# Kernel optimization log

Hardware: AMD Instinct MI355X
Metric: run time of the kernel (lower is better)

Reference implementation:

```python
import jax, jax.numpy as jnp
import numpy as np

N, E = 50000, 600000
D_IN, HID, CLS = 128, 128, 64
TEM = (0.9, 0.8)  # tem[0], tem[1] from init


def setup_inputs() -> dict:
    key = jax.random.key(0)
    ks = jax.random.split(key, 20)
    def lin(k, fan_in, shape):
        return (jax.random.normal(k, shape, jnp.float32) / np.float32(np.sqrt(fan_in)))
    return {
        "features": jax.random.normal(ks[0], (N, D_IN), jnp.float32),
        "src1": jax.random.randint(ks[1], (E,), 0, N, jnp.int32),
        "dst1": jax.random.randint(ks[2], (E,), 0, N, jnp.int32),
        "src2": jax.random.randint(ks[3], (E,), 0, N, jnp.int32),
        "dst2": jax.random.randint(ks[4], (E,), 0, N, jnp.int32),
        "W1": lin(ks[5], D_IN, (D_IN, HID)),
        "b1": jnp.zeros((HID,), jnp.float32),
        "W2": lin(ks[6], HID, (HID, CLS)),
        "b2": jnp.zeros((CLS,), jnp.float32),
        "Wg11": lin(ks[7], 2 * HID, (2 * HID, 1)),
        "bg11": jnp.zeros((1,), jnp.float32),
        "Wg12": lin(ks[8], 2 * HID, (2 * HID, 1)),
        "bg12": jnp.zeros((1,), jnp.float32),
        "Wg21": lin(ks[9], 2 * CLS, (2 * CLS, 1)),
        "bg21": jnp.zeros((1,), jnp.float32),
        "Wg22": lin(ks[10], 2 * CLS, (2 * CLS, 1)),
        "bg22": jnp.zeros((1,), jnp.float32),
    }


def _gin(x, src, dst, W, b):
    # DGL GINConv, aggregator='sum', eps=0: apply_func(x + sum_{u->v} x_u)
    agg = jax.ops.segment_sum(x[src], dst, num_segments=N)  # [N, d]
    return (x + agg) @ W + b


def _gate_scale(a, c, Wg, bg):
    # ga = softmax(Linear(cat[a,c]), dim=1): [N,1] -> all ones (size-1 axis)
    # torch.diag of [N,1] matrix -> its single diagonal element [0,0]
    g = jnp.concatenate([a, c], axis=1) @ Wg + bg  # [N, 1]
    g = jax.nn.softmax(g, axis=1)
    return g[0, 0]  # scalar (dropout is identity in eval mode)


def reference(features, src1, dst1, src2, dst2, W1, b1, W2, b2,
              Wg11, bg11, Wg12, bg12, Wg21, bg21, Wg22, bg22):
    # layer 1 on both graphs (no ELU in the two-graph branch, per source)
    x11 = _gin(features, src1, dst1, W1, b1)
    x12 = _gin(features, src2, dst2, W1, b1)
    x12 = TEM[1] * _gate_scale(x11, x12, Wg11, bg11) * x12
    x11 = TEM[0] * _gate_scale(x12, x11, Wg12, bg12) * x11
    x1 = x11 + x12
    # layer 2 on both graphs
    x21 = _gin(x1, src1, dst1, W2, b2)
    x22 = _gin(x1, src2, dst2, W2, b2)
    x22 = TEM[1] * _gate_scale(x21, x22, Wg21, bg21) * x22
    x21 = TEM[0] * _gate_scale(x22, x21, Wg22, bg22) * x21
    return x21 + x22
```

## Files before the change

kernel.cpp:

```cpp
#include <hip/hip_runtime.h>

#define N_NODES 50000
#define N_EDGES 600000
#define D 128
#define NCLS 64

#define BIN_SHIFT 9
#define BIN_ROWS 512
#define NBINS 196
#define BIN_CAP 8192
#define CHUNK 4096
#define EPT (CHUNK / 256)
#define NCHUNKS 293
#define W12_BLOCKS 17

__device__ inline unsigned short f2bf(float f) {
  unsigned int u = __float_as_uint(f);
  unsigned int r = (u + 0x7FFF + ((u >> 16) & 1)) >> 16;
  return (unsigned short)r;
}
__device__ inline float bf2f(unsigned short b) {
  return __uint_as_float(((unsigned int)b) << 16);
}


__global__ __launch_bounds__(256) void scatter_w12(const int* __restrict__ src1,
                                                   const int* __restrict__ dst1,
                                                   const int* __restrict__ src2,
                                                   const int* __restrict__ dst2,
                                                   int* __restrict__ bincnt,
                                                   int2* __restrict__ binbuf,
                                                   const float* __restrict__ W1,
                                                   const float* __restrict__ W2,
                                                   const float* __restrict__ b1,
                                                   float* __restrict__ W12,
                                                   float* __restrict__ cvec) {
  __shared__ int bcnt[NBINS];
  __shared__ int boff[NBINS];
  __shared__ int gbase[NBINS];
  __shared__ int stmp[256];
  __shared__ int2 stage[CHUNK];

  if (blockIdx.x >= NCHUNKS) {
    int gid = (blockIdx.x - NCHUNKS) * 256 + threadIdx.x;
    for (int t = gid; t < D * NCLS + NCLS; t += W12_BLOCKS * 256) {
      if (t < D * NCLS) {
        int i = t >> 6, j = t & 63;
        float s = 0.f;
        for (int k = 0; k < D; ++k) s += W1[i * D + k] * W2[k * NCLS + j];
        W12[t] = s;
      } else {
        int j = t - D * NCLS;
        float s = 0.f;
        for (int k = 0; k < D; ++k) s += b1[k] * W2[k * NCLS + j];
        cvec[j] = s;
      }
    }
    return;
  }

  int base = blockIdx.x * CHUNK;
  int nloc = min(CHUNK, 2 * N_EDGES - base);

  for (int t = threadIdx.x; t < NBINS; t += 256) bcnt[t] = 0;
  __syncthreads();

  int rows[EPT], srcs[EPT], bins[EPT];
#pragma unroll
  for (int k = 0; k < EPT; ++k) {
    int t = threadIdx.x + k * 256;
    rows[k] = -1;
    if (t < nloc) {
      int i = base + t;
      int row, sv;
      if (i < N_EDGES) { row = dst1[i]; sv = src1[i]; }
      else { int e = i - N_EDGES; row = N_NODES + dst2[e]; sv = src2[e]; }
      rows[k] = row; srcs[k] = sv;
      bins[k] = row >> BIN_SHIFT;
      atomicAdd(&bcnt[bins[k]], 1);
    }
  }
  __syncthreads();
  {
    int tid = threadIdx.x;
    int v = (tid < NBINS) ? bcnt[tid] : 0;
    stmp[tid] = v;
    __syncthreads();
    int x = v;
    for (int o = 1; o < 256; o <<= 1) {
      int y = (tid >= o) ? stmp[tid - o] : 0;
      __syncthreads();
      x += y;
      stmp[tid] = x;
      __syncthreads();
    }
    if (tid < NBINS) boff[tid] = x - v;
  }
  __syncthreads();
  for (int t = threadIdx.x; t < NBINS; t += 256) {
    gbase[t] = bcnt[t];
    bcnt[t] = boff[t];
  }
  __syncthreads();
#pragma unroll
  for (int k = 0; k < EPT; ++k) {
    if (rows[k] >= 0) {
      int p = atomicAdd(&bcnt[bins[k]], 1);
      stage[p] = make_int2(rows[k], srcs[k]);
    }
  }
  __syncthreads();
  for (int t = threadIdx.x; t < NBINS; t += 256) {
    int c = gbase[t];
    if (c > 0) gbase[t] = atomicAdd(&bincnt[t], c);
  }
  __syncthreads();
  for (int j = threadIdx.x; j < nloc; j += 256) {
    int2 e = stage[j];
    int b = e.x >> BIN_SHIFT;
    int gp = gbase[b] + (j - boff[b]);
    if (gp < BIN_CAP) binbuf[(size_t)b * BIN_CAP + gp] = e;
  }
}


__global__ __launch_bounds__(512) void build_gemm(const int* __restrict__ bincnt,
                                                  const int2* __restrict__ binbuf,
                                                  int* __restrict__ off, int* __restrict__ adj,
                                                  const float* __restrict__ A,
                                                  const float* __restrict__ W,
                                                  unsigned short* __restrict__ C) {
  __shared__ int sh[BIN_ROWS];
  __shared__ int lp[BIN_ROWS];
  __shared__ int stmp[256];
  __shared__ float As[16][65];
  __shared__ float Ws[16][64];

  int tid = threadIdx.x;

  if (blockIdx.x < NBINS) {
    int b = blockIdx.x;
    if (tid < 256) stmp[tid] = (tid < NBINS) ? bincnt[tid] : 0;
    __syncthreads();
    int x = (tid < 256) ? stmp[tid] : 0;
    for (int o = 1; o < 256; o <<= 1) {
      int y = (tid < 256 && tid >= o) ? stmp[tid - o] : 0;
      __syncthreads();
      x += y;
      if (tid < 256) stmp[tid] = x;
      __syncthreads();
    }
    int base = (b == 0) ? 0 : stmp[b - 1];
    if (b == 0 && tid == 0) off[2 * N_NODES] = stmp[NBINS - 1];
    int n = min(bincnt[b], BIN_CAP);

    sh[tid] = 0;
    __syncthreads();
    for (int t = tid; t < n; t += 512) {
      int row = binbuf[(size_t)b * BIN_CAP + t].x;
      atomicAdd(&sh[row & (BIN_ROWS - 1)], 1);
    }
    __syncthreads();
    int v = sh[tid];
    int xx = v;
    for (int o = 1; o < BIN_ROWS; o <<= 1) {
      int y = (tid >= o) ? sh[tid - o] : 0;
      __syncthreads();
      xx += y;
      sh[tid] = xx;
      __syncthreads();
    }
    lp[tid] = xx - v;
    int row = (b << BIN_SHIFT) + tid;
    if (row < 2 * N_NODES) off[row] = base + lp[tid];
    __syncthreads();
    sh[tid] = lp[tid];
    __syncthreads();
    for (int t = tid; t < n; t += 512) {
      int2 e = binbuf[(size_t)b * BIN_CAP + t];
      int p = atomicAdd(&sh[e.x & (BIN_ROWS - 1)], 1);
      adj[base + p] = e.y;
    }
    return;
  }

  constexpr int BM = 64, BK = 16, BN = 64;
  constexpr int TCOL = BN / 16;
  const int tx = tid & 15;
  const int ty = (tid >> 4) & 15;
  const int row0 = (blockIdx.x - NBINS) * BM;
  float acc[4][TCOL];
#pragma unroll
  for (int r = 0; r < 4; ++r)
#pragma unroll
    for (int c = 0; c < TCOL; ++c) acc[r][c] = 0.f;

  for (int k0 = 0; k0 < D; k0 += BK) {
    if (tid < 256) {
      int r = tid >> 2;
      int kq = (tid & 3) << 2;
      int gr = row0 + r;
      float4 v = make_float4(0.f, 0.f, 0.f, 0.f);
      if (gr < N_NODES) v = *(const float4*)(A + (size_t)gr * D + k0 + kq);
      As[kq + 0][r] = v.x;
      As[kq + 1][r] = v.y;
      As[kq + 2][r] = v.z;
      As[kq + 3][r] = v.w;
    }
    if (tid < 256) {
      int k = tid >> 4;
      int c4 = (tid & 15) << 2;
      *(float4*)(&Ws[k][c4]) = *(const float4*)(W + (size_t)(k0 + k) * BN + c4);
    }
    __syncthreads();
    if (tid < 256) {
#pragma unroll
      for (int k = 0; k < BK; ++k) {
        float a[4];
#pragma unroll
        for (int r = 0; r < 4; ++r) a[r] = As[k][ty * 4 + r];
        float w[TCOL];
#pragma unroll
        for (int c = 0; c < TCOL; ++c) w[c] = Ws[k][tx * TCOL + c];
#pragma unroll
        for (int r = 0; r < 4; ++r)
#pragma unroll
          for (int c = 0; c < TCOL; ++c) acc[r][c] += a[r] * w[c];
      }
    }
    __syncthreads();
  }
  if (tid < 256) {
#pragma unroll
    for (int r = 0; r < 4; ++r) {
      int gr = row0 + ty * 4 + r;
      if (gr < N_NODES) {
        ushort4 pk;
        pk.x = f2bf(acc[r][0]);
        pk.y = f2bf(acc[r][1]);
        pk.z = f2bf(acc[r][2]);
        pk.w = f2bf(acc[r][3]);
        *(ushort4*)(C + (size_t)gr * BN + tx * TCOL) = pk;
      }
    }
  }
}


template <int FIN, int OUT_BF16>
__global__ __launch_bounds__(256) void agg64_kernel(const unsigned short* __restrict__ X,
                                                    const int* __restrict__ off,
                                                    const int* __restrict__ adj,
                                                    const float* __restrict__ cvec,
                                                    const float* __restrict__ b2,
                                                    void* __restrict__ Yv) {
  int wid = (blockIdx.x * blockDim.x + threadIdx.x) >> 6;
  if (wid >= N_NODES) return;
  int lane = threadIdx.x & 63;

  float self = bf2f(X[(size_t)wid * 64 + lane]);

  int s1 = off[wid], e1 = off[wid + 1];
  int s2 = off[N_NODES + wid], e2 = off[N_NODES + wid + 1];

  float acc[2];
#pragma unroll
  for (int g = 0; g < 2; ++g) {
    int s = g ? s2 : s1, e = g ? e2 : e1;
    float a0 = 0.f, a1 = 0.f, a2 = 0.f, a3 = 0.f;
    for (int base = s; base < e; base += 64) {
      int m = e - base;
      if (m > 64) m = 64;
      int idx = (lane < m) ? adj[base + lane] : 0;
      int i = 0;
      for (; i + 4 <= m; i += 4) {
        int n0 = __shfl(idx, i + 0);
        int n1 = __shfl(idx, i + 1);
        int n2 = __shfl(idx, i + 2);
        int n3 = __shfl(idx, i + 3);
        float f0 = bf2f(X[(size_t)n0 * 64 + lane]);
        float f1 = bf2f(X[(size_t)n1 * 64 + lane]);
        float f2 = bf2f(X[(size_t)n2 * 64 + lane]);
        float f3 = bf2f(X[(size_t)n3 * 64 + lane]);
        a0 += f0; a1 += f1; a2 += f2; a3 += f3;
      }
      for (; i < m; ++i) {
        int n0 = __shfl(idx, i);
        a0 += bf2f(X[(size_t)n0 * 64 + lane]);
      }
    }
    acc[g] = (a0 + a1) + (a2 + a3);
  }
  float y = 1.7f * self + 0.9f * acc[0] + 0.8f * acc[1];
  if (FIN) {
    float sv = 1.7f * (1.7f + 0.9f * (float)(e1 - s1) + 0.8f * (float)(e2 - s2));
    y += sv * cvec[lane] + 1.7f * b2[lane];
  }
  if (OUT_BF16) {
    ((unsigned short*)Yv)[(size_t)wid * 64 + lane] = f2bf(y);
  } else {
    ((float*)Yv)[(size_t)wid * 64 + lane] = y;
  }
}


extern "C" void kernel_launch(void* const* d_in, const int* in_sizes, int n_in,
                              void* d_out, int out_size, void* d_ws, size_t ws_size,
                              hipStream_t stream) {
  const float* F  = (const float*)d_in[0];
  const int* src1 = (const int*)d_in[1];
  const int* dst1 = (const int*)d_in[2];
  const int* src2 = (const int*)d_in[3];
  const int* dst2 = (const int*)d_in[4];
  const float* W1 = (const float*)d_in[5];
  const float* b1 = (const float*)d_in[6];
  const float* W2 = (const float*)d_in[7];
  const float* b2 = (const float*)d_in[8];
  float* out = (float*)d_out;

  char* ws = (char*)d_ws;
  auto aln = [](size_t x) { return (x + 255) & ~(size_t)255; };
  size_t o = 0;
  int* bincnt  = (int*)(ws + o); o = aln(o + (size_t)NBINS * 4);
  int* off     = (int*)(ws + o); o = aln(o + ((size_t)2 * N_NODES + 1) * 4);
  int2* binbuf = (int2*)(ws + o); o = aln(o + (size_t)NBINS * BIN_CAP * 8);
  int* adj     = (int*)(ws + o); o = aln(o + (size_t)2 * N_EDGES * 4);
  float* W12   = (float*)(ws + o); o = aln(o + (size_t)D * NCLS * 4);
  float* cvec  = (float*)(ws + o); o = aln(o + NCLS * 4);
  unsigned short* H = (unsigned short*)(ws + o); o = aln(o + (size_t)N_NODES * NCLS * 2);
  unsigned short* T = (unsigned short*)(ws + o); o = aln(o + (size_t)N_NODES * NCLS * 2);
  (void)ws_size;

  hipMemsetAsync(bincnt, 0, (size_t)NBINS * 4, stream);
  scatter_w12<<<NCHUNKS + W12_BLOCKS, 256, 0, stream>>>(src1, dst1, src2, dst2,
                                                        bincnt, binbuf, W1, W2, b1, W12, cvec);
  build_gemm<<<NBINS + (N_NODES + 63) / 64, 512, 0, stream>>>(bincnt, binbuf, off, adj,
                                                              F, W12, H);
  agg64_kernel<0, 1><<<N_NODES / 4, 256, 0, stream>>>(H, off, adj, cvec, b2, T);
  agg64_kernel<1, 0><<<N_NODES / 4, 256, 0, stream>>>(T, off, adj, cvec, b2, out);
}
```

Baseline: 211.2 us.

## Interleave graph CSR rows per node and merge aggregation loops

```diff
diff --git a/kernel.cpp b/kernel.cpp
--- a/kernel.cpp
+++ b/kernel.cpp
@@ -73,8 +73,8 @@
     if (t < nloc) {
       int i = base + t;
       int row, sv;
-      if (i < N_EDGES) { row = dst1[i]; sv = src1[i]; }
-      else { int e = i - N_EDGES; row = N_NODES + dst2[e]; sv = src2[e]; }
+      if (i < N_EDGES) { row = dst1[i] * 2; sv = src1[i]; }
+      else { int e = i - N_EDGES; row = dst2[e] * 2 + 1; sv = src2[e]; }
       rows[k] = row; srcs[k] = sv;
       bins[k] = row >> BIN_SHIFT;
       atomicAdd(&bcnt[bins[k]], 1);
@@ -260,40 +260,51 @@
 
   float self = bf2f(X[(size_t)wid * 64 + lane]);
 
-  int s1 = off[wid], e1 = off[wid + 1];
-  int s2 = off[N_NODES + wid], e2 = off[N_NODES + wid + 1];
-
-  float acc[2];
-#pragma unroll
-  for (int g = 0; g < 2; ++g) {
-    int s = g ? s2 : s1, e = g ? e2 : e1;
-    float a0 = 0.f, a1 = 0.f, a2 = 0.f, a3 = 0.f;
-    for (int base = s; base < e; base += 64) {
-      int m = e - base;
-      if (m > 64) m = 64;
-      int idx = (lane < m) ? adj[base + lane] : 0;
-      int i = 0;
-      for (; i + 4 <= m; i += 4) {
-        int n0 = __shfl(idx, i + 0);
-        int n1 = __shfl(idx, i + 1);
-        int n2 = __shfl(idx, i + 2);
-        int n3 = __shfl(idx, i + 3);
-        float f0 = bf2f(X[(size_t)n0 * 64 + lane]);
-        float f1 = bf2f(X[(size_t)n1 * 64 + lane]);
-        float f2 = bf2f(X[(size_t)n2 * 64 + lane]);
-        float f3 = bf2f(X[(size_t)n3 * 64 + lane]);
-        a0 += f0; a1 += f1; a2 += f2; a3 += f3;
-      }
-      for (; i < m; ++i) {
-        int n0 = __shfl(idx, i);
-        a0 += bf2f(X[(size_t)n0 * 64 + lane]);
-      }
-    }
-    acc[g] = (a0 + a1) + (a2 + a3);
-  }
-  float y = 1.7f * self + 0.9f * acc[0] + 0.8f * acc[1];
+  int s = off[2 * wid], mid = off[2 * wid + 1], e = off[2 * wid + 2];
+
+  float a0 = 0.f, a1 = 0.f, a2 = 0.f, a3 = 0.f;
+  float a4 = 0.f, a5 = 0.f, a6 = 0.f, a7 = 0.f;
+  for (int base = s; base < e; base += 64) {
+    int m = e - base;
+    if (m > 64) m = 64;
+    int idx = (lane < m) ? adj[base + lane] : 0;
+    int i = 0;
+    for (; i + 8 <= m; i += 8) {
+      int n0 = __shfl(idx, i + 0);
+      int n1 = __shfl(idx, i + 1);
+      int n2 = __shfl(idx, i + 2);
+      int n3 = __shfl(idx, i + 3);
+      int n4 = __shfl(idx, i + 4);
+      int n5 = __shfl(idx, i + 5);
+      int n6 = __shfl(idx, i + 6);
+      int n7 = __shfl(idx, i + 7);
+      float w0 = (base + i + 0 < mid) ? 0.9f : 0.8f;
+      float w1 = (base + i + 1 < mid) ? 0.9f : 0.8f;
+      float w2 = (base + i + 2 < mid) ? 0.9f : 0.8f;
+      float w3 = (base + i + 3 < mid) ? 0.9f : 0.8f;
+      float w4 = (base + i + 4 < mid) ? 0.9f : 0.8f;
+      float w5 = (base + i + 5 < mid) ? 0.9f : 0.8f;
+      float w6 = (base + i + 6 < mid) ? 0.9f : 0.8f;
+      float w7 = (base + i + 7 < mid) ? 0.9f : 0.8f;
+      a0 += w0 * bf2f(X[(size_t)n0 * 64 + lane]);
+      a1 += w1 * bf2f(X[(size_t)n1 * 64 + lane]);
+      a2 += w2 * bf2f(X[(size_t)n2 * 64 + lane]);
+      a3 += w3 * bf2f(X[(size_t)n3 * 64 + lane]);
+      a4 += w4 * bf2f(X[(size_t)n4 * 64 + lane]);
+      a5 += w5 * bf2f(X[(size_t)n5 * 64 + lane]);
+      a6 += w6 * bf2f(X[(size_t)n6 * 64 + lane]);
+      a7 += w7 * bf2f(X[(size_t)n7 * 64 + lane]);
+    }
+    for (; i < m; ++i) {
+      int n0 = __shfl(idx, i);
+      float w = (base + i < mid) ? 0.9f : 0.8f;
+      a0 += w * bf2f(X[(size_t)n0 * 64 + lane]);
+    }
+  }
+  float acc = ((a0 + a1) + (a2 + a3)) + ((a4 + a5) + (a6 + a7));
+  float y = 1.7f * self + acc;
   if (FIN) {
-    float sv = 1.7f * (1.7f + 0.9f * (float)(e1 - s1) + 0.8f * (float)(e2 - s2));
+    float sv = 1.7f * (1.7f + 0.9f * (float)(mid - s) + 0.8f * (float)(e - mid));
     y += sv * cvec[lane] + 1.7f * b2[lane];
   }
   if (OUT_BF16) {
```

Result: faster. 206.1 us (-2.4%).
